# Kernel optimization log

Hardware: AMD Instinct MI355X
Metric: run time of the kernel (lower is better)

## Reference

```python
import jax, jax.numpy as jnp
import numpy as np

B, M, H, D, K, V = 32, 4096, 32, 4096, 128, 128

def setup_inputs() -> dict:
    key = jax.random.key(0)
    ks = jax.random.split(key, 7)
    s = lambda fan: 1.0 / np.sqrt(fan)
    return {
        "x": jax.random.normal(ks[0], (B, D), jnp.float32),
        "K_prev": jax.random.normal(ks[1], (B, M, K), jnp.float32),
        "V_prev": jax.random.normal(ks[2], (B, M, V), jnp.float32),
        "P_q": jax.random.normal(ks[3], (H, D, K), jnp.float32) * s(D),
        "P_k": jax.random.normal(ks[4], (D, K), jnp.float32) * s(D),
        "P_v": jax.random.normal(ks[5], (D, V), jnp.float32) * s(D),
        "P_o": jax.random.normal(ks[6], (H, D, V), jnp.float32) * s(D),
    }

def reference(x, K_prev, V_prev, P_q, P_k, P_v, P_o):
    # per-head query projection: [b,d] x [h,d,k] -> [b,h,k]
    q = jnp.einsum('bd,hdk->bhk', x, P_q)
    # shared (multi-query) K/V projection of the new token, appended to cache
    k_new = jnp.einsum('bd,dk->bk', x, P_k)          # [b,k]
    v_new = jnp.einsum('bd,dv->bv', x, P_v)          # [b,v]
    K_new = jnp.concatenate([K_prev, k_new[:, None, :]], axis=1)  # [b,m+1,k]
    V_new = jnp.concatenate([V_prev, v_new[:, None, :]], axis=1)  # [b,m+1,v]
    # attention over shared cache
    logits = jnp.einsum('bhk,bmk->bhm', q, K_new)    # [b,h,m+1]
    w = jax.nn.softmax(logits, axis=-1)
    o = jnp.einsum('bhm,bmv->bhv', w, V_new)         # [b,h,v]
    y = jnp.einsum('bhv,hdv->bd', o, P_o)            # [b,d]
    return (y, K_new, V_new)
```

## Files before the change

### kernel.cpp

```cpp
#include <hip/hip_runtime.h>

#define B_ 32
#define M_ 4096
#define M1_ 4097
#define H_ 32
#define D_ 4096

typedef float float4_ __attribute__((ext_vector_type(4)));
typedef float f32x4 __attribute__((ext_vector_type(4)));
typedef short short8 __attribute__((ext_vector_type(8)));
typedef short short4_ __attribute__((ext_vector_type(4)));

#define KOFF 131072
#define VOFF 16912384

#define Q_OFF     0u
#define O_OFF     139264u
#define YPART_OFF 270336u
#define QPART_OFF 1318912u
#define APO_OFF   1318912u
#define MSUM_OFF  5513216u

__device__ __forceinline__ unsigned short f2bf(float f) {
  union { float f; unsigned u; } cv; cv.f = f;
  return (unsigned short)((cv.u + 0x7FFFu + ((cv.u >> 16) & 1u)) >> 16);
}
__device__ __forceinline__ float bf2f(unsigned short b) {
  union { unsigned u; float f; } cv; cv.u = ((unsigned)b) << 16;
  return cv.f;
}
__device__ __forceinline__ short8 pack8(const float* t) {
  short8 r;
#pragma unroll
  for (int j = 0; j < 8; ++j) r[j] = (short)f2bf(t[j]);
  return r;
}
__device__ __forceinline__ short8 load8cvt(const float* __restrict__ p) {
  float t[8];
  float4_ v0 = *(const float4_*)p;
  float4_ v1 = *(const float4_*)(p + 4);
#pragma unroll
  for (int j = 0; j < 4; ++j) { t[j] = v0[j]; t[4 + j] = v1[j]; }
  return pack8(t);
}

__global__ __launch_bounds__(256) void k_proj(const float* __restrict__ x,
    const float* __restrict__ Pq, const float* __restrict__ Pk,
    const float* __restrict__ Pv, float* __restrict__ qpart)
{
  int bid = blockIdx.x;
  int hh = bid >> 4;
  int c  = bid & 15;
  const float* W = (hh < 32) ? (Pq + (size_t)hh * D_ * 128)
                             : ((hh == 32) ? Pk : Pv);
  int d0 = c * 256;
  int tid = threadIdx.x;
  int w = tid >> 6, l = tid & 63, l15 = l & 15, lg = l >> 4;
  f32x4 acc[2][2] = {};
  for (int ks = 0; ks < 8; ++ks) {
    int dk = d0 + ks * 32 + lg * 8;
    short8 af[2];
#pragma unroll
    for (int bt = 0; bt < 2; ++bt)
      af[bt] = load8cvt(x + (size_t)(bt * 16 + l15) * D_ + dk);
    short8 bf[2];
#pragma unroll
    for (int nti = 0; nti < 2; ++nti) {
      int col = (2 * w + nti) * 16 + l15;
      float t[8];
#pragma unroll
      for (int j = 0; j < 8; ++j) t[j] = W[(size_t)(dk + j) * 128 + col];
      bf[nti] = pack8(t);
    }
#pragma unroll
    for (int bt = 0; bt < 2; ++bt)
#pragma unroll
      for (int nti = 0; nti < 2; ++nti)
        acc[bt][nti] = __builtin_amdgcn_mfma_f32_16x16x32_bf16(af[bt], bf[nti], acc[bt][nti], 0, 0, 0);
  }
#pragma unroll
  for (int bt = 0; bt < 2; ++bt)
#pragma unroll
    for (int nti = 0; nti < 2; ++nti) {
      int k = (2 * w + nti) * 16 + l15;
#pragma unroll
      for (int i = 0; i < 4; ++i) {
        int b = bt * 16 + lg * 4 + i;
        qpart[(size_t)((c * 34 + hh) * 32 + b) * 128 + k] = acc[bt][nti][i];
      }
    }
}

__global__ __launch_bounds__(256) void k_reduce_q(const float* __restrict__ qpart,
    float* __restrict__ q, float* __restrict__ dout)
{
  int idx = blockIdx.x * 256 + threadIdx.x;
  if (idx >= 34 * 32 * 128) return;
  float s = 0.f;
#pragma unroll
  for (int cc = 0; cc < 16; ++cc) s += qpart[(size_t)cc * 139264 + idx];
  q[idx] = s;
  int hh = idx >> 12;
  if (hh >= 32) {
    int b = (idx >> 7) & 31, k = idx & 127;
    size_t off = (hh == 32) ? (size_t)KOFF : (size_t)VOFF;
    dout[off + ((size_t)b * M1_ + M_) * 128 + k] = s;
  }
}

__global__ __launch_bounds__(256, 8) void k_attn(const float* __restrict__ Kp,
    const float* __restrict__ Vp, const float* __restrict__ q,
    float* __restrict__ dout, unsigned short* __restrict__ apo,
    float* __restrict__ msum)
{
  __shared__ float S[32][73];
  __shared__ unsigned short P[32][64];
  __shared__ float smax[32], ssum[32], sextra[32];
  int bid = blockIdx.x;
  int b = bid >> 6, c = bid & 63;
  int m0 = c * 64;
  int tid = threadIdx.x, w = tid >> 6, l = tid & 63, l15 = l & 15, lg = l >> 4;
  const float* Kt = Kp + ((size_t)b * M_ + m0) * 128;
  const float* Vt = Vp + ((size_t)b * M_ + m0) * 128;
  float* Kn = dout + KOFF + ((size_t)b * M1_ + m0) * 128;
  float* Vn = dout + VOFF + ((size_t)b * M1_ + m0) * 128;

#pragma unroll
  for (int g = 0; g < 2; ++g) {
    float4_ t[4];
#pragma unroll
    for (int i = 0; i < 4; ++i) t[i] = ((const float4_*)Kt)[tid + (g * 4 + i) * 256];
    __builtin_amdgcn_sched_barrier(0);
#pragma unroll
    for (int i = 0; i < 4; ++i)
      __builtin_nontemporal_store(t[i], &((float4_*)Kn)[tid + (g * 4 + i) * 256]);
  }
#pragma unroll
  for (int g = 0; g < 2; ++g) {
    float4_ t[4];
#pragma unroll
    for (int i = 0; i < 4; ++i) t[i] = ((const float4_*)Vt)[tid + (g * 4 + i) * 256];
    __builtin_amdgcn_sched_barrier(0);
#pragma unroll
    for (int i = 0; i < 4; ++i)
      __builtin_nontemporal_store(t[i], &((float4_*)Vn)[tid + (g * 4 + i) * 256]);
  }

  f32x4 sacc[2] = {};
#pragma unroll
  for (int ks = 0; ks < 4; ++ks) {
    short8 bfK = load8cvt(Kt + (size_t)(w * 16 + l15) * 128 + ks * 32 + lg * 8);
#pragma unroll
    for (int ht = 0; ht < 2; ++ht) {
      short8 af = load8cvt(q + (size_t)((ht * 16 + l15) * 32 + b) * 128 + ks * 32 + lg * 8);
      sacc[ht] = __builtin_amdgcn_mfma_f32_16x16x32_bf16(af, bfK, sacc[ht], 0, 0, 0);
    }
  }
#pragma unroll
  for (int ht = 0; ht < 2; ++ht)
#pragma unroll
    for (int i = 0; i < 4; ++i)
      S[ht * 16 + lg * 4 + i][w * 16 + l15] = sacc[ht][i];

  if (c == 63 && tid < 32) {
    int h = tid;
    const float* qh = q + (size_t)(h * 32 + b) * 128;
    const float* kn = q + (size_t)(32 * 32 + b) * 128;
    float s = 0.f;
    for (int k = 0; k < 128; ++k) s += qh[k] * kn[k];
    S[h][64] = s;
  }
  __syncthreads();

  {
    int h = tid >> 3, i = tid & 7;
    float vals[8];
    float mx = -3e38f;
#pragma unroll
    for (int j = 0; j < 8; ++j) { vals[j] = S[h][i * 8 + j]; mx = fmaxf(mx, vals[j]); }
#pragma unroll
    for (int d = 1; d < 8; d <<= 1) mx = fmaxf(mx, __shfl_xor(mx, d));
    if (c == 63) mx = fmaxf(mx, S[h][64]);
    float se = 0.f;
    short8 pw;
#pragma unroll
    for (int j = 0; j < 8; ++j) {
      float p = __expf(vals[j] - mx);
      se += p;
      pw[j] = (short)f2bf(p);
    }
    *(short8*)((char*)P + h * 128 + ((i * 16) ^ ((h & 7) << 4))) = pw;
    if (c == 63 && i == 0) { float pe = __expf(S[h][64] - mx); se += pe; sextra[h] = pe; }
#pragma unroll
    for (int d = 1; d < 8; d <<= 1) se += __shfl_xor(se, d);
    if (i == 0) { smax[h] = mx; ssum[h] = se; }
  }
  __syncthreads();

  f32x4 oacc[2][2] = {};
#pragma unroll
  for (int ksv = 0; ksv < 2; ++ksv) {
    short8 af[2];
#pragma unroll
    for (int ht = 0; ht < 2; ++ht) {
      int h = ht * 16 + l15;
      af[ht] = *(const short8*)((const char*)P + h * 128 + ((ksv * 64 + lg * 16) ^ ((h & 7) << 4)));
    }
    short8 bf[2];
#pragma unroll
    for (int vti = 0; vti < 2; ++vti) {
      int v = w * 32 + vti * 16 + l15;
      float t[8];
#pragma unroll
      for (int j = 0; j < 8; ++j) t[j] = Vt[(size_t)(ksv * 32 + lg * 8 + j) * 128 + v];
      bf[vti] = pack8(t);
    }
#pragma unroll
    for (int ht = 0; ht < 2; ++ht)
#pragma unroll
      for (int vti = 0; vti < 2; ++vti)
        oacc[ht][vti] = __builtin_amdgcn_mfma_f32_16x16x32_bf16(af[ht], bf[vti], oacc[ht][vti], 0, 0, 0);
  }

  const float* vnew = q + (size_t)(33 * 32 + b) * 128;
#pragma unroll
  for (int ht = 0; ht < 2; ++ht)
#pragma unroll
    for (int vti = 0; vti < 2; ++vti) {
      int v = w * 32 + vti * 16 + l15;
#pragma unroll
      for (int i = 0; i < 4; ++i) {
        int h = ht * 16 + lg * 4 + i;
        float val = oacc[ht][vti][i];
        if (c == 63) val += sextra[h] * vnew[v];
        apo[((size_t)(b * 64 + c) * 32 + h) * 128 + v] = f2bf(val);
      }
    }
  if (tid < 32) {
    size_t base = ((size_t)(b * 64 + c) * 32 + tid) * 2;
    msum[base]     = smax[tid];
    msum[base + 1] = ssum[tid];
  }
}

__global__ __launch_bounds__(256) void k_combine(const unsigned short* __restrict__ apo,
    const float* __restrict__ msum, float* __restrict__ o)
{
  __shared__ float redN[4][128];
  __shared__ float redD[4];
  int bid = blockIdx.x;
  int b = bid >> 5, h = bid & 31;
  int tid = threadIdx.x, w = tid >> 6, l = tid & 63;

  float gm = msum[((size_t)(b * 64 + l) * 32 + h) * 2];
#pragma unroll
  for (int d = 1; d < 64; d <<= 1) gm = fmaxf(gm, __shfl_xor(gm, d));

  float num0 = 0.f, num1 = 0.f, den = 0.f;
#pragma unroll 4
  for (int i = 0; i < 16; ++i) {
    int cc = w * 16 + i;
    size_t slot = (size_t)(b * 64 + cc) * 32 + h;
    float sc = __expf(msum[slot * 2] - gm);
    den += sc * msum[slot * 2 + 1];
    unsigned pp = *(const unsigned*)&apo[slot * 128 + l * 2];
    num0 += sc * bf2f((unsigned short)(pp & 0xFFFFu));
    num1 += sc * bf2f((unsigned short)(pp >> 16));
  }
  redN[w][l * 2] = num0;
  redN[w][l * 2 + 1] = num1;
  if (l == 0) redD[w] = den;
  __syncthreads();
  if (tid < 128) {
    float num = redN[0][tid] + redN[1][tid] + redN[2][tid] + redN[3][tid];
    float dd  = redD[0] + redD[1] + redD[2] + redD[3];
    o[((size_t)(b * 32 + h)) * 128 + tid] = num / dd;
  }
}

__global__ __launch_bounds__(256) void k_out(const float* __restrict__ o,
    const float* __restrict__ Po, float* __restrict__ ypart)
{
  int bid = blockIdx.x;
  int dt = bid >> 3, hg = bid & 7;
  int tid = threadIdx.x, w = tid >> 6, l = tid & 63, l15 = l & 15, lg = l >> 4;
  int d = dt * 64 + w * 16 + l15;
  f32x4 acc[2] = {};
  for (int hi = 0; hi < 4; ++hi) {
    int h = hg * 4 + hi;
#pragma unroll
    for (int ks = 0; ks < 4; ++ks) {
      short8 af[2];
#pragma unroll
      for (int bt = 0; bt < 2; ++bt)
        af[bt] = load8cvt(o + ((size_t)((bt * 16 + l15) * 32 + h)) * 128 + ks * 32 + lg * 8);
      short8 bf = load8cvt(Po + ((size_t)h * D_ + d) * 128 + ks * 32 + lg * 8);
#pragma unroll
      for (int bt = 0; bt < 2; ++bt)
        acc[bt] = __builtin_amdgcn_mfma_f32_16x16x32_bf16(af[bt], bf, acc[bt], 0, 0, 0);
    }
  }
#pragma unroll
  for (int bt = 0; bt < 2; ++bt)
#pragma unroll
    for (int i = 0; i < 4; ++i) {
      int b = bt * 16 + lg * 4 + i;
      ypart[((size_t)(hg * 32 + b)) * 4096 + d] = acc[bt][i];
    }
}

__global__ __launch_bounds__(256) void k_reduce_y(const float* __restrict__ ypart,
    float* __restrict__ dout)
{
  int idx = blockIdx.x * 256 + threadIdx.x;
  float s = 0.f;
#pragma unroll
  for (int g = 0; g < 8; ++g) s += ypart[(size_t)g * 131072 + idx];
  dout[idx] = s;
}

extern "C" void kernel_launch(void* const* d_in, const int* in_sizes, int n_in,
                              void* d_out, int out_size, void* d_ws, size_t ws_size,
                              hipStream_t stream) {
  (void)in_sizes; (void)n_in; (void)out_size; (void)ws_size;
  const float* x  = (const float*)d_in[0];
  const float* Kp = (const float*)d_in[1];
  const float* Vp = (const float*)d_in[2];
  const float* Pq = (const float*)d_in[3];
  const float* Pk = (const float*)d_in[4];
  const float* Pv = (const float*)d_in[5];
  const float* Po = (const float*)d_in[6];
  float* out = (float*)d_out;
  float* ws  = (float*)d_ws;
  float* q     = ws + Q_OFF;
  float* o     = ws + O_OFF;
  float* ypart = ws + YPART_OFF;
  float* qpart = ws + QPART_OFF;
  unsigned short* apo = (unsigned short*)(ws + APO_OFF);
  float* msum  = ws + MSUM_OFF;

  hipLaunchKernelGGL(k_proj,     dim3(544),  dim3(256), 0, stream, x, Pq, Pk, Pv, qpart);
  hipLaunchKernelGGL(k_reduce_q, dim3(544),  dim3(256), 0, stream, qpart, q, out);
  hipLaunchKernelGGL(k_attn,     dim3(2048), dim3(256), 0, stream, Kp, Vp, q, out, apo, msum);
  hipLaunchKernelGGL(k_combine,  dim3(1024), dim3(256), 0, stream, apo, msum, o);
  hipLaunchKernelGGL(k_out,      dim3(512),  dim3(256), 0, stream, o, Po, ypart);
  hipLaunchKernelGGL(k_reduce_y, dim3(512),  dim3(256), 0, stream, ypart, out);
}
```

Measured before the change: 131.9 us.

## Reuse copied K/V tiles in registers and LDS instead of reloading from global

The attention kernel used to copy K and V tiles to the output cache and then reload them from global memory for the QK and PV MFMAs. Now each thread loads its K row slice once into registers, writes it out, and packs it to bf16 for the QK MFMA directly. V is staged as bf16 in a new LDS tile for the PV step instead of strided global reads. The extra registers and 16KB of LDS lower the occupancy hint from 8 to 4 waves, and nontemporal stores become regular stores.

```diff
diff --git a/kernel.cpp b/kernel.cpp
--- a/kernel.cpp
+++ b/kernel.cpp
@@ -108,11 +108,12 @@
   }
 }
 
-__global__ __launch_bounds__(256, 8) void k_attn(const float* __restrict__ Kp,
+__global__ __launch_bounds__(256, 4) void k_attn(const float* __restrict__ Kp,
     const float* __restrict__ Vp, const float* __restrict__ q,
     float* __restrict__ dout, unsigned short* __restrict__ apo,
     float* __restrict__ msum)
 {
+  __shared__ unsigned short Vl[64][128];
   __shared__ float S[32][73];
   __shared__ unsigned short P[32][64];
   __shared__ float smax[32], ssum[32], sextra[32];
@@ -125,35 +126,49 @@
   float* Kn = dout + KOFF + ((size_t)b * M1_ + m0) * 128;
   float* Vn = dout + VOFF + ((size_t)b * M1_ + m0) * 128;
 
-#pragma unroll
-  for (int g = 0; g < 2; ++g) {
-    float4_ t[4];
-#pragma unroll
-    for (int i = 0; i < 4; ++i) t[i] = ((const float4_*)Kt)[tid + (g * 4 + i) * 256];
-    __builtin_amdgcn_sched_barrier(0);
-#pragma unroll
-    for (int i = 0; i < 4; ++i)
-      __builtin_nontemporal_store(t[i], &((float4_*)Kn)[tid + (g * 4 + i) * 256]);
-  }
-#pragma unroll
-  for (int g = 0; g < 2; ++g) {
-    float4_ t[4];
-#pragma unroll
-    for (int i = 0; i < 4; ++i) t[i] = ((const float4_*)Vt)[tid + (g * 4 + i) * 256];
-    __builtin_amdgcn_sched_barrier(0);
-#pragma unroll
-    for (int i = 0; i < 4; ++i)
-      __builtin_nontemporal_store(t[i], &((float4_*)Vn)[tid + (g * 4 + i) * 256]);
+  const float* Krow = Kt + (size_t)(w * 16 + l15) * 128;
+  float4_ kr[8], vr[8];
+#pragma unroll
+  for (int ks = 0; ks < 4; ++ks) {
+    kr[2 * ks]     = *(const float4_*)(Krow + ks * 32 + lg * 8);
+    kr[2 * ks + 1] = *(const float4_*)(Krow + ks * 32 + lg * 8 + 4);
+  }
+#pragma unroll
+  for (int i = 0; i < 8; ++i) vr[i] = ((const float4_*)Vt)[tid + i * 256];
+  __builtin_amdgcn_sched_barrier(0);
+
+  float* Knrow = Kn + (size_t)(w * 16 + l15) * 128;
+#pragma unroll
+  for (int ks = 0; ks < 4; ++ks) {
+    *(float4_*)(Knrow + ks * 32 + lg * 8)     = kr[2 * ks];
+    *(float4_*)(Knrow + ks * 32 + lg * 8 + 4) = kr[2 * ks + 1];
+  }
+#pragma unroll
+  for (int i = 0; i < 8; ++i) {
+    int idx = tid + i * 256;
+    ((float4_*)Vn)[idx] = vr[i];
+    int m = idx >> 5, v = (idx & 31) * 4;
+    short4_ s;
+#pragma unroll
+    for (int j = 0; j < 4; ++j) s[j] = (short)f2bf(vr[i][j]);
+    *(short4_*)&Vl[m][v] = s;
+  }
+  short8 kf[4];
+#pragma unroll
+  for (int ks = 0; ks < 4; ++ks) {
+    float t[8];
+#pragma unroll
+    for (int j = 0; j < 4; ++j) { t[j] = kr[2 * ks][j]; t[4 + j] = kr[2 * ks + 1][j]; }
+    kf[ks] = pack8(t);
   }
 
   f32x4 sacc[2] = {};
 #pragma unroll
   for (int ks = 0; ks < 4; ++ks) {
-    short8 bfK = load8cvt(Kt + (size_t)(w * 16 + l15) * 128 + ks * 32 + lg * 8);
 #pragma unroll
     for (int ht = 0; ht < 2; ++ht) {
       short8 af = load8cvt(q + (size_t)((ht * 16 + l15) * 32 + b) * 128 + ks * 32 + lg * 8);
-      sacc[ht] = __builtin_amdgcn_mfma_f32_16x16x32_bf16(af, bfK, sacc[ht], 0, 0, 0);
+      sacc[ht] = __builtin_amdgcn_mfma_f32_16x16x32_bf16(af, kf[ks], sacc[ht], 0, 0, 0);
     }
   }
 #pragma unroll
@@ -210,10 +225,10 @@
 #pragma unroll
     for (int vti = 0; vti < 2; ++vti) {
       int v = w * 32 + vti * 16 + l15;
-      float t[8];
-#pragma unroll
-      for (int j = 0; j < 8; ++j) t[j] = Vt[(size_t)(ksv * 32 + lg * 8 + j) * 128 + v];
-      bf[vti] = pack8(t);
+      short8 t;
+#pragma unroll
+      for (int j = 0; j < 8; ++j) t[j] = (short)Vl[ksv * 32 + lg * 8 + j][v];
+      bf[vti] = t;
     }
 #pragma unroll
     for (int ht = 0; ht < 2; ++ht)
```

New measurement: 137.8 us. 1.04x slower.

## Restructure attention into per-wave online-softmax with double-buffered async V loads

Applied to the files above, without the earlier changes.

The attention kernel is rewritten so each wave processes 64 cache rows as four 16-row chunks. It uses an online softmax and double-buffers K in registers and V in LDS through global_load_lds, with explicit vmcnt waits to overlap loads, cache copy-out and MFMA work. The block-level LDS syncs and the separate copy loops go away, the new-token contribution moves into the combine kernel, and the projection split-K doubles to 32 chunks. This cuts the block count to 512 with launch bounds 2, which risks lower occupancy, and the hand-counted vmcnt values are fragile.

```diff
diff --git a/kernel.cpp b/kernel.cpp
--- a/kernel.cpp
+++ b/kernel.cpp
@@ -19,7 +19,10 @@
 #define YPART_OFF 270336u
 #define QPART_OFF 1318912u
 #define APO_OFF   1318912u
-#define MSUM_OFF  5513216u
+#define MSUM_OFF  5775360u
+
+#define WAITV(n) asm volatile("s_waitcnt vmcnt(" #n ")" ::: "memory")
+#define SBAR() __builtin_amdgcn_sched_barrier(0)
 
 __device__ __forceinline__ unsigned short f2bf(float f) {
   union { float f; unsigned u; } cv; cv.f = f;
@@ -43,21 +46,26 @@
   for (int j = 0; j < 4; ++j) { t[j] = v0[j]; t[4 + j] = v1[j]; }
   return pack8(t);
 }
+__device__ __forceinline__ void load_lds16(const float* g, float* l) {
+  __builtin_amdgcn_global_load_lds(
+      (const __attribute__((address_space(1))) unsigned int*)g,
+      (__attribute__((address_space(3))) unsigned int*)l, 16, 0, 0);
+}
 
 __global__ __launch_bounds__(256) void k_proj(const float* __restrict__ x,
     const float* __restrict__ Pq, const float* __restrict__ Pk,
     const float* __restrict__ Pv, float* __restrict__ qpart)
 {
   int bid = blockIdx.x;
-  int hh = bid >> 4;
-  int c  = bid & 15;
+  int hh = bid >> 5;
+  int c  = bid & 31;
   const float* W = (hh < 32) ? (Pq + (size_t)hh * D_ * 128)
                              : ((hh == 32) ? Pk : Pv);
-  int d0 = c * 256;
+  int d0 = c * 128;
   int tid = threadIdx.x;
   int w = tid >> 6, l = tid & 63, l15 = l & 15, lg = l >> 4;
   f32x4 acc[2][2] = {};
-  for (int ks = 0; ks < 8; ++ks) {
+  for (int ks = 0; ks < 4; ++ks) {
     int dk = d0 + ks * 32 + lg * 8;
     short8 af[2];
 #pragma unroll
@@ -98,7 +106,7 @@
   if (idx >= 34 * 32 * 128) return;
   float s = 0.f;
 #pragma unroll
-  for (int cc = 0; cc < 16; ++cc) s += qpart[(size_t)cc * 139264 + idx];
+  for (int cc = 0; cc < 32; ++cc) s += qpart[(size_t)cc * 139264 + idx];
   q[idx] = s;
   int hh = idx >> 12;
   if (hh >= 32) {
@@ -108,143 +116,181 @@
   }
 }
 
-__global__ __launch_bounds__(256, 8) void k_attn(const float* __restrict__ Kp,
+#define ISSUE(T, KR, VB) do { \
+  const float* Kc_ = Kb + (T) * 16 * 128; \
+  const float* Vc_ = Vb + (T) * 16 * 128; \
+  const float* Krow_ = Kc_ + (size_t)l15 * 128; \
+  _Pragma("unroll") \
+  for (int ks = 0; ks < 4; ++ks) { \
+    KR[2 * ks]     = *(const float4_*)(Krow_ + ks * 32 + lg * 8); \
+    KR[2 * ks + 1] = *(const float4_*)(Krow_ + ks * 32 + lg * 8 + 4); \
+  } \
+  _Pragma("unroll") \
+  for (int i = 0; i < 8; ++i) load_lds16(Vc_ + i * 256 + l * 4, VB + i * 256); \
+} while (0)
+
+#define DO_CHUNK(T, KR, VB) do { \
+   \
+  float* Knrow_ = Knb + (T) * 16 * 128 + (size_t)l15 * 128; \
+  _Pragma("unroll") \
+  for (int ks = 0; ks < 4; ++ks) { \
+    *(float4_*)(Knrow_ + ks * 32 + lg * 8)     = KR[2 * ks]; \
+    *(float4_*)(Knrow_ + ks * 32 + lg * 8 + 4) = KR[2 * ks + 1]; \
+  } \
+   \
+  float* Vnc_ = Vnb + (T) * 16 * 128; \
+  _Pragma("unroll") \
+  for (int i = 0; i < 8; ++i) { \
+    float4_ t_ = *(const float4_*)(VB + (i * 64 + l) * 4); \
+    *(float4_*)(Vnc_ + (size_t)(i * 64 + l) * 4) = t_; \
+  } \
+   \
+  short8 kf_[4]; \
+  _Pragma("unroll") \
+  for (int ks = 0; ks < 4; ++ks) { \
+    float tt_[8]; \
+    _Pragma("unroll") \
+    for (int j = 0; j < 4; ++j) { tt_[j] = KR[2 * ks][j]; tt_[4 + j] = KR[2 * ks + 1][j]; } \
+    kf_[ks] = pack8(tt_); \
+  } \
+   \
+  f32x4 sacc_[2] = {}; \
+  _Pragma("unroll") \
+  for (int ks = 0; ks < 4; ++ks) \
+    _Pragma("unroll") \
+    for (int ht = 0; ht < 2; ++ht) \
+      sacc_[ht] = __builtin_amdgcn_mfma_f32_16x16x32_bf16(af[ht][ks], kf_[ks], sacc_[ht], 0, 0, 0); \
+   \
+  _Pragma("unroll") \
+  for (int ht = 0; ht < 2; ++ht) { \
+    f32x4 mx_; \
+    _Pragma("unroll") \
+    for (int i = 0; i < 4; ++i) { \
+      float v_ = sacc_[ht][i]; \
+      v_ = fmaxf(v_, __shfl_xor(v_, 1)); v_ = fmaxf(v_, __shfl_xor(v_, 2)); \
+      v_ = fmaxf(v_, __shfl_xor(v_, 4)); v_ = fmaxf(v_, __shfl_xor(v_, 8)); \
+      mx_[i] = v_; \
+    } \
+    f32x4 fsc_; \
+    _Pragma("unroll") \
+    for (int i = 0; i < 4; ++i) { \
+      float mn_ = fmaxf(mrun[ht][i], mx_[i]); \
+      fsc_[i] = __expf(mrun[ht][i] - mn_); \
+      mrun[ht][i] = mn_; \
+    } \
+    _Pragma("unroll") \
+    for (int vt = 0; vt < 8; ++vt) oacc[ht][vt] *= fsc_; \
+    _Pragma("unroll") \
+    for (int i = 0; i < 4; ++i) { \
+      float p_ = __expf(sacc_[ht][i] - mrun[ht][i]); \
+      lsum[ht][i] = lsum[ht][i] * fsc_[i] + p_; \
+      Plds[w][ht * 16 + lg * 4 + i][l15] = f2bf(p_); \
+    } \
+  } \
+  asm volatile("" ::: "memory"); \
+   \
+  short8 z_ = {}; \
+  short8 pa_[2]; \
+  _Pragma("unroll") \
+  for (int ht = 0; ht < 2; ++ht) \
+    pa_[ht] = (lg < 2) ? *(const short8*)&Plds[w][ht * 16 + l15][lg * 8] : z_; \
+  _Pragma("unroll") \
+  for (int vt = 0; vt < 8; ++vt) { \
+    short8 bfv_ = z_; \
+    if (lg < 2) { \
+      float t_[8]; \
+      _Pragma("unroll") \
+      for (int j = 0; j < 8; ++j) t_[j] = VB[(lg * 8 + j) * 128 + vt * 16 + l15]; \
+      bfv_ = pack8(t_); \
+    } \
+    _Pragma("unroll") \
+    for (int ht = 0; ht < 2; ++ht) \
+      oacc[ht][vt] = __builtin_amdgcn_mfma_f32_16x16x32_bf16(pa_[ht], bfv_, oacc[ht][vt], 0, 0, 0); \
+  } \
+} while (0)
+
+__global__ __launch_bounds__(256, 2) void k_attn(const float* __restrict__ Kp,
     const float* __restrict__ Vp, const float* __restrict__ q,
     float* __restrict__ dout, unsigned short* __restrict__ apo,
     float* __restrict__ msum)
 {
-  __shared__ float S[32][73];
-  __shared__ unsigned short P[32][64];
-  __shared__ float smax[32], ssum[32], sextra[32];
+  __shared__ float Vbuf[4][2][2048];
+  __shared__ unsigned short Plds[4][32][16];
   int bid = blockIdx.x;
-  int b = bid >> 6, c = bid & 63;
-  int m0 = c * 64;
+  int b = bid >> 4;
   int tid = threadIdx.x, w = tid >> 6, l = tid & 63, l15 = l & 15, lg = l >> 4;
-  const float* Kt = Kp + ((size_t)b * M_ + m0) * 128;
-  const float* Vt = Vp + ((size_t)b * M_ + m0) * 128;
-  float* Kn = dout + KOFF + ((size_t)b * M1_ + m0) * 128;
-  float* Vn = dout + VOFF + ((size_t)b * M1_ + m0) * 128;
-
-#pragma unroll
-  for (int g = 0; g < 2; ++g) {
-    float4_ t[4];
-#pragma unroll
-    for (int i = 0; i < 4; ++i) t[i] = ((const float4_*)Kt)[tid + (g * 4 + i) * 256];
-    __builtin_amdgcn_sched_barrier(0);
-#pragma unroll
-    for (int i = 0; i < 4; ++i)
-      __builtin_nontemporal_store(t[i], &((float4_*)Kn)[tid + (g * 4 + i) * 256]);
-  }
-#pragma unroll
-  for (int g = 0; g < 2; ++g) {
-    float4_ t[4];
-#pragma unroll
-    for (int i = 0; i < 4; ++i) t[i] = ((const float4_*)Vt)[tid + (g * 4 + i) * 256];
-    __builtin_amdgcn_sched_barrier(0);
-#pragma unroll
-    for (int i = 0; i < 4; ++i)
-      __builtin_nontemporal_store(t[i], &((float4_*)Vn)[tid + (g * 4 + i) * 256]);
-  }
-
-  f32x4 sacc[2] = {};
-#pragma unroll
-  for (int ks = 0; ks < 4; ++ks) {
-    short8 bfK = load8cvt(Kt + (size_t)(w * 16 + l15) * 128 + ks * 32 + lg * 8);
-#pragma unroll
-    for (int ht = 0; ht < 2; ++ht) {
-      short8 af = load8cvt(q + (size_t)((ht * 16 + l15) * 32 + b) * 128 + ks * 32 + lg * 8);
-      sacc[ht] = __builtin_amdgcn_mfma_f32_16x16x32_bf16(af, bfK, sacc[ht], 0, 0, 0);
+  int wid = (bid & 15) * 4 + w;
+  const float* Kb = Kp + ((size_t)b * M_ + wid * 64) * 128;
+  const float* Vb = Vp + ((size_t)b * M_ + wid * 64) * 128;
+  float* Knb = dout + KOFF + ((size_t)b * M1_ + wid * 64) * 128;
+  float* Vnb = dout + VOFF + ((size_t)b * M1_ + wid * 64) * 128;
+  float* vb0 = &Vbuf[w][0][0];
+  float* vb1 = &Vbuf[w][1][0];
+
+  short8 af[2][4];
+#pragma unroll
+  for (int ks = 0; ks < 4; ++ks)
+#pragma unroll
+    for (int ht = 0; ht < 2; ++ht)
+      af[ht][ks] = load8cvt(q + (size_t)((ht * 16 + l15) * 32 + b) * 128 + ks * 32 + lg * 8);
+
+  float4_ krA[8], krB[8];
+  f32x4 mrun[2], lsum[2], oacc[2][8];
+#pragma unroll
+  for (int ht = 0; ht < 2; ++ht) {
+#pragma unroll
+    for (int i = 0; i < 4; ++i) { mrun[ht][i] = -3e38f; lsum[ht][i] = 0.f; }
+#pragma unroll
+    for (int vt = 0; vt < 8; ++vt) oacc[ht][vt] = f32x4{0.f, 0.f, 0.f, 0.f};
+  }
+
+  ISSUE(0, krA, vb0); SBAR();
+  ISSUE(1, krB, vb1); SBAR();
+  WAITV(16); SBAR();
+  DO_CHUNK(0, krA, vb0);
+  ISSUE(2, krA, vb0); SBAR();
+  WAITV(32); SBAR();
+  DO_CHUNK(1, krB, vb1);
+  ISSUE(3, krB, vb1); SBAR();
+  WAITV(32); SBAR();
+  DO_CHUNK(2, krA, vb0);
+  WAITV(16); SBAR();
+  DO_CHUNK(3, krB, vb1);
+
+#pragma unroll
+  for (int ht = 0; ht < 2; ++ht)
+#pragma unroll
+    for (int i = 0; i < 4; ++i) {
+      float s = lsum[ht][i];
+      s += __shfl_xor(s, 1); s += __shfl_xor(s, 2);
+      s += __shfl_xor(s, 4); s += __shfl_xor(s, 8);
+      lsum[ht][i] = s;
     }
-  }
-#pragma unroll
-  for (int ht = 0; ht < 2; ++ht)
-#pragma unroll
-    for (int i = 0; i < 4; ++i)
-      S[ht * 16 + lg * 4 + i][w * 16 + l15] = sacc[ht][i];
-
-  if (c == 63 && tid < 32) {
-    int h = tid;
-    const float* qh = q + (size_t)(h * 32 + b) * 128;
-    const float* kn = q + (size_t)(32 * 32 + b) * 128;
-    float s = 0.f;
-    for (int k = 0; k < 128; ++k) s += qh[k] * kn[k];
-    S[h][64] = s;
-  }
-  __syncthreads();
-
-  {
-    int h = tid >> 3, i = tid & 7;
-    float vals[8];
-    float mx = -3e38f;
-#pragma unroll
-    for (int j = 0; j < 8; ++j) { vals[j] = S[h][i * 8 + j]; mx = fmaxf(mx, vals[j]); }
-#pragma unroll
-    for (int d = 1; d < 8; d <<= 1) mx = fmaxf(mx, __shfl_xor(mx, d));
-    if (c == 63) mx = fmaxf(mx, S[h][64]);
-    float se = 0.f;
-    short8 pw;
-#pragma unroll
-    for (int j = 0; j < 8; ++j) {
-      float p = __expf(vals[j] - mx);
-      se += p;
-      pw[j] = (short)f2bf(p);
-    }
-    *(short8*)((char*)P + h * 128 + ((i * 16) ^ ((h & 7) << 4))) = pw;
-    if (c == 63 && i == 0) { float pe = __expf(S[h][64] - mx); se += pe; sextra[h] = pe; }
-#pragma unroll
-    for (int d = 1; d < 8; d <<= 1) se += __shfl_xor(se, d);
-    if (i == 0) { smax[h] = mx; ssum[h] = se; }
-  }
-  __syncthreads();
-
-  f32x4 oacc[2][2] = {};
-#pragma unroll
-  for (int ksv = 0; ksv < 2; ++ksv) {
-    short8 af[2];
-#pragma unroll
-    for (int ht = 0; ht < 2; ++ht) {
-      int h = ht * 16 + l15;
-      af[ht] = *(const short8*)((const char*)P + h * 128 + ((ksv * 64 + lg * 16) ^ ((h & 7) << 4)));
-    }
-    short8 bf[2];
-#pragma unroll
-    for (int vti = 0; vti < 2; ++vti) {
-      int v = w * 32 + vti * 16 + l15;
-      float t[8];
-#pragma unroll
-      for (int j = 0; j < 8; ++j) t[j] = Vt[(size_t)(ksv * 32 + lg * 8 + j) * 128 + v];
-      bf[vti] = pack8(t);
-    }
+  size_t slot = (size_t)(b * 64 + wid) * 32;
+  if (l15 == 0) {
 #pragma unroll
     for (int ht = 0; ht < 2; ++ht)
-#pragma unroll
-      for (int vti = 0; vti < 2; ++vti)
-        oacc[ht][vti] = __builtin_amdgcn_mfma_f32_16x16x32_bf16(af[ht], bf[vti], oacc[ht][vti], 0, 0, 0);
-  }
-
-  const float* vnew = q + (size_t)(33 * 32 + b) * 128;
-#pragma unroll
-  for (int ht = 0; ht < 2; ++ht)
-#pragma unroll
-    for (int vti = 0; vti < 2; ++vti) {
-      int v = w * 32 + vti * 16 + l15;
 #pragma unroll
       for (int i = 0; i < 4; ++i) {
         int h = ht * 16 + lg * 4 + i;
-        float val = oacc[ht][vti][i];
-        if (c == 63) val += sextra[h] * vnew[v];
-        apo[((size_t)(b * 64 + c) * 32 + h) * 128 + v] = f2bf(val);
+        msum[(slot + h) * 2]     = mrun[ht][i];
+        msum[(slot + h) * 2 + 1] = lsum[ht][i];
       }
-    }
-  if (tid < 32) {
-    size_t base = ((size_t)(b * 64 + c) * 32 + tid) * 2;
-    msum[base]     = smax[tid];
-    msum[base + 1] = ssum[tid];
-  }
+  }
+#pragma unroll
+  for (int ht = 0; ht < 2; ++ht)
+#pragma unroll
+    for (int vt = 0; vt < 8; ++vt)
+#pragma unroll
+      for (int i = 0; i < 4; ++i) {
+        int h = ht * 16 + lg * 4 + i;
+        int v = vt * 16 + l15;
+        apo[(slot + h) * 128 + v] = f2bf(oacc[ht][vt][i]);
+      }
 }
 
 __global__ __launch_bounds__(256) void k_combine(const unsigned short* __restrict__ apo,
-    const float* __restrict__ msum, float* __restrict__ o)
+    const float* __restrict__ msum, const float* __restrict__ q, float* __restrict__ o)
 {
   __shared__ float redN[4][128];
   __shared__ float redD[4];
@@ -252,9 +298,18 @@
   int b = bid >> 5, h = bid & 31;
   int tid = threadIdx.x, w = tid >> 6, l = tid & 63;
 
+  const float* qh = q + (size_t)(h * 32 + b) * 128;
+  const float* kn = q + (size_t)(1024 + b) * 128;
+  const float* vn = q + (size_t)(1056 + b) * 128;
+  float e = qh[2 * l] * kn[2 * l] + qh[2 * l + 1] * kn[2 * l + 1];
+#pragma unroll
+  for (int d = 1; d < 64; d <<= 1) e += __shfl_xor(e, d);
+
   float gm = msum[((size_t)(b * 64 + l) * 32 + h) * 2];
 #pragma unroll
   for (int d = 1; d < 64; d <<= 1) gm = fmaxf(gm, __shfl_xor(gm, d));
+  gm = fmaxf(gm, e);
+  float pe = __expf(e - gm);
 
   float num0 = 0.f, num1 = 0.f, den = 0.f;
 #pragma unroll 4
@@ -269,10 +324,10 @@
   }
   redN[w][l * 2] = num0;
   redN[w][l * 2 + 1] = num1;
-  if (l == 0) redD[w] = den;
+  if (l == 0) redD[w] = den + (w == 0 ? pe : 0.f);
   __syncthreads();
   if (tid < 128) {
-    float num = redN[0][tid] + redN[1][tid] + redN[2][tid] + redN[3][tid];
+    float num = redN[0][tid] + redN[1][tid] + redN[2][tid] + redN[3][tid] + pe * vn[tid];
     float dd  = redD[0] + redD[1] + redD[2] + redD[3];
     o[((size_t)(b * 32 + h)) * 128 + tid] = num / dd;
   }
@@ -339,10 +394,10 @@
   unsigned short* apo = (unsigned short*)(ws + APO_OFF);
   float* msum  = ws + MSUM_OFF;
 
-  hipLaunchKernelGGL(k_proj,     dim3(544),  dim3(256), 0, stream, x, Pq, Pk, Pv, qpart);
+  hipLaunchKernelGGL(k_proj,     dim3(1088), dim3(256), 0, stream, x, Pq, Pk, Pv, qpart);
   hipLaunchKernelGGL(k_reduce_q, dim3(544),  dim3(256), 0, stream, qpart, q, out);
-  hipLaunchKernelGGL(k_attn,     dim3(2048), dim3(256), 0, stream, Kp, Vp, q, out, apo, msum);
-  hipLaunchKernelGGL(k_combine,  dim3(1024), dim3(256), 0, stream, apo, msum, o);
+  hipLaunchKernelGGL(k_attn,     dim3(512),  dim3(256), 0, stream, Kp, Vp, q, out, apo, msum);
+  hipLaunchKernelGGL(k_combine,  dim3(1024), dim3(256), 0, stream, apo, msum, q, o);
   hipLaunchKernelGGL(k_out,      dim3(512),  dim3(256), 0, stream, o, Po, ypart);
   hipLaunchKernelGGL(k_reduce_y, dim3(512),  dim3(256), 0, stream, ypart, out);
 }
```

Measured after the change: 135.0 us. 2.4% more time.
